# Optimization experiments

Measured on AMD Instinct MI355X. Metric: run time of the kernel, lower is better.

Reference implementation:

```python
import jax, jax.numpy as jnp
import numpy as np

# Mamba config (HF defaults for hidden_size=256)
VOCAB = 4096
H = 256          # hidden_size
I = 512          # intermediate_size = 2*H
N = 16           # state_size
R = 16           # time_step_rank = ceil(H/16)
K = 4            # conv_kernel
NUM_LAYERS = 4
B, L = 4, 1024
EPS = 1e-5


def _rmsnorm(x, w):
    return x * jax.lax.rsqrt(jnp.mean(x * x, axis=-1, keepdims=True) + EPS) * w


def setup_inputs() -> dict:
    key = jax.random.key(0)
    ks = jax.random.split(key, 20)
    s = 0.02
    Lyr = NUM_LAYERS
    inp = {
        'input_ids': jax.random.randint(ks[0], (B, L), 0, VOCAB),
        'lengths': jax.random.randint(ks[1], (B,), 1, L + 1),
        'embed': jax.random.normal(ks[2], (VOCAB, H)) * s,
        'norm_w': jnp.ones((Lyr, H)),
        'in_proj_w': jax.random.normal(ks[3], (Lyr, 2 * I, H)) * s,
        'conv_w': jax.random.normal(ks[4], (Lyr, I, K)) * s,
        'conv_b': jnp.zeros((Lyr, I)),
        'x_proj_w': jax.random.normal(ks[5], (Lyr, R + 2 * N, I)) * s,
        'dt_proj_w': jax.random.normal(ks[6], (Lyr, I, R)) * s,
        'dt_proj_b': jax.random.normal(ks[7], (Lyr, I)) * 0.5 - 4.0,
        'A_log': jnp.log(jnp.broadcast_to(jnp.arange(1, N + 1, dtype=jnp.float32), (Lyr, I, N))),
        'D': jnp.ones((Lyr, I)),
        'out_proj_w': jax.random.normal(ks[8], (Lyr, H, I)) * s,
        'final_norm_w': jnp.ones((H,)),
        'head_w1': jax.random.normal(ks[9], (H // 4, H)) * s,
        'head_b1': jnp.zeros((H // 4,)),
        'head_w2': jax.random.normal(ks[10], (1, H // 4)) * s,
        'head_b2': jnp.zeros((1,)),
    }
    return inp


def _mixer(x, in_proj_w, conv_w, conv_b, x_proj_w, dt_proj_w, dt_proj_b, A_log, D_, out_proj_w):
    b, l, _ = x.shape
    proj = x @ in_proj_w.T                      # (b,l,2I)
    xs, gate = proj[..., :I], proj[..., I:]
    # depthwise causal conv1d (kernel K, left pad K-1)
    xp = jnp.pad(xs, ((0, 0), (K - 1, 0), (0, 0)))
    conv = sum(xp[:, k:k + l, :] * conv_w[:, k] for k in range(K))
    xs = jax.nn.silu(conv + conv_b)             # (b,l,I)
    ssm = xs @ x_proj_w.T                       # (b,l,R+2N)
    dt_r, Bmat, Cmat = ssm[..., :R], ssm[..., R:R + N], ssm[..., R + N:]
    dt = jax.nn.softplus(dt_r @ dt_proj_w.T + dt_proj_b)   # (b,l,I)
    A = -jnp.exp(A_log)                         # (I,N)
    dA = jnp.exp(dt[..., None] * A)             # (b,l,I,N)
    dBu = (dt * xs)[..., None] * Bmat[:, :, None, :]        # (b,l,I,N)

    def step(state, inputs):
        a_t, bu_t, c_t = inputs                 # (b,I,N),(b,I,N),(b,N)
        state = a_t * state + bu_t
        y = jnp.einsum('bdn,bn->bd', state, c_t)
        return state, y

    state0 = jnp.zeros((b, I, N), dtype=x.dtype)
    _, ys = jax.lax.scan(step, state0, (dA.transpose(1, 0, 2, 3),
                                        dBu.transpose(1, 0, 2, 3),
                                        Cmat.transpose(1, 0, 2)))
    ys = ys.transpose(1, 0, 2)                  # (b,l,I)
    y = (ys + xs * D_) * jax.nn.silu(gate)
    return y @ out_proj_w.T                     # (b,l,H)


def reference(input_ids, lengths, embed, norm_w, in_proj_w, conv_w, conv_b,
              x_proj_w, dt_proj_w, dt_proj_b, A_log, D, out_proj_w,
              final_norm_w, head_w1, head_b1, head_w2, head_b2):
    h = embed[input_ids]                        # (B,L,H)
    for i in range(NUM_LAYERS):
        res = h
        x = _rmsnorm(h, norm_w[i])
        h = res + _mixer(x, in_proj_w[i], conv_w[i], conv_b[i], x_proj_w[i],
                         dt_proj_w[i], dt_proj_b[i], A_log[i], D[i], out_proj_w[i])
    h = _rmsnorm(h, final_norm_w)
    pooled = h[jnp.arange(h.shape[0]), lengths - 1]         # (B,H)
    hd = jax.nn.gelu(pooled @ head_w1.T + head_b1, approximate=False)
    out = hd @ head_w2.T + head_b2
    return out.squeeze(-1)                      # (B,)
```

## Files before the change

kernel.cpp:

```cpp
#include <hip/hip_runtime.h>
#include <hip/hip_bf16.h>

#define HDIM 256
#define IDIM 512
#define NST 16
#define KCONV 4
#define LAYERS 4
#define BATCH 4
#define LSEQ 1024
#define TOK (BATCH * LSEQ)

typedef unsigned short u16;
typedef float f32x4 __attribute__((ext_vector_type(4)));
typedef short bf16x8 __attribute__((ext_vector_type(8)));

static __device__ __forceinline__ u16 f2bf(float f) {
    __hip_bfloat16 h = __float2bfloat16(f);
    return reinterpret_cast<u16&>(h);
}
static __device__ __forceinline__ float bf2f(u16 b) {
    return __builtin_bit_cast(float, (unsigned)b << 16);
}
static __device__ __forceinline__ float bfup(uint2 u, int j) {
    unsigned w = (j < 2) ? u.x : u.y;
    unsigned bits = (j & 1) ? (w & 0xffff0000u) : (w << 16);
    return __builtin_bit_cast(float, bits);
}

#define DPP_ROW_ADD(p, CTRL)                                                   \
    p += __builtin_bit_cast(float, __builtin_amdgcn_update_dpp(                \
             0, __builtin_bit_cast(int, p), CTRL, 0xf, 0xf, false))

__global__ __launch_bounds__(256) void embed_kernel(const int* __restrict__ ids,
                                                    const float* __restrict__ embed,
                                                    float* __restrict__ h) {
    int idx = blockIdx.x * 256 + threadIdx.x;
    if (idx < TOK * HDIM) {
        int tok = idx >> 8;
        int c = idx & (HDIM - 1);
        h[idx] = embed[ids[tok] * HDIM + c];
    }
}

__global__ __launch_bounds__(256) void cvt4_bf16_kernel(const float* __restrict__ s0, u16* __restrict__ d0,
                                                        const float* __restrict__ s1, u16* __restrict__ d1,
                                                        const float* __restrict__ s2, u16* __restrict__ d2,
                                                        const float* __restrict__ s3, u16* __restrict__ d3) {
    const float* in;
    u16* out;
    int base;
    int bid = blockIdx.x;
    if (bid < 1024)      { in = s0; out = d0; base = bid; }
    else if (bid < 1536) { in = s1; out = d1; base = bid - 1024; }
    else if (bid < 1632) { in = s2; out = d2; base = bid - 1536; }
    else                 { in = s3; out = d3; base = bid - 1632; }
    int j = (base * 256 + threadIdx.x) * 4;
    float4 v = *(const float4*)&in[j];
    unsigned lo = (unsigned)f2bf(v.x) | ((unsigned)f2bf(v.y) << 16);
    unsigned hi = (unsigned)f2bf(v.z) | ((unsigned)f2bf(v.w) << 16);
    *(uint2*)&out[j] = make_uint2(lo, hi);
}

__global__ __launch_bounds__(256) void rmsnorm_kernel(const float* __restrict__ h,
                                                      const float* __restrict__ w,
                                                      u16* __restrict__ xb) {
    int wid = threadIdx.x >> 6, lane = threadIdx.x & 63;
    int tok = blockIdx.x * 4 + wid;
    float4 v = *(const float4*)&h[(size_t)tok * HDIM + lane * 4];
    float s = v.x * v.x + v.y * v.y + v.z * v.z + v.w * v.w;
    #pragma unroll
    for (int m = 32; m >= 1; m >>= 1) s += __shfl_xor(s, m, 64);
    float rstd = rsqrtf(s * (1.0f / HDIM) + 1e-5f);
    float4 wv = *(const float4*)&w[lane * 4];
    unsigned lo = (unsigned)f2bf(v.x * rstd * wv.x) | ((unsigned)f2bf(v.y * rstd * wv.y) << 16);
    unsigned hi = (unsigned)f2bf(v.z * rstd * wv.z) | ((unsigned)f2bf(v.w * rstd * wv.w) << 16);
    *(uint2*)&xb[(size_t)tok * HDIM + lane * 4] = make_uint2(lo, hi);
}

template <int EPI>
__global__ __launch_bounds__(256) void gemm_bf16_kernel(const u16* __restrict__ A,
                                                        const u16* __restrict__ W,
                                                        float* __restrict__ C,
                                                        int M, int N, int K) {
    const int BM = 128, BK = 32;
    __shared__ __align__(16) u16 Al[BM][BK + 8];
    __shared__ __align__(16) u16 Bl[BM][BK + 8];
    int m0 = blockIdx.y * BM, n0 = blockIdx.x * BM;
    int tid = threadIdx.x;
    int lane = tid & 63;
    int wid = tid >> 6;
    int wr = wid >> 1, wc = wid & 1;
    int r = lane & 15, g = lane >> 4;

    f32x4 acc[4][4] = {};

    int srow = tid & 127;
    const u16* src = (tid < 128) ? (A + (size_t)(m0 + srow) * K)
                                 : (W + (size_t)(n0 + srow) * K);
    u16* dstrow = (tid < 128) ? &Al[srow][0] : &Bl[srow][0];

    for (int k0 = 0; k0 < K; k0 += BK) {
        uint4 v0 = *(const uint4*)(src + k0);
        uint4 v1 = *(const uint4*)(src + k0 + 8);
        uint4 v2 = *(const uint4*)(src + k0 + 16);
        uint4 v3 = *(const uint4*)(src + k0 + 24);
        __syncthreads();
        *(uint4*)(dstrow)      = v0;
        *(uint4*)(dstrow + 8)  = v1;
        *(uint4*)(dstrow + 16) = v2;
        *(uint4*)(dstrow + 24) = v3;
        __syncthreads();

        bf16x8 af[4], bfr[4];
        #pragma unroll
        for (int f = 0; f < 4; ++f) {
            af[f]  = *(const bf16x8*)&Al[wr * 64 + f * 16 + r][g * 8];
            bfr[f] = *(const bf16x8*)&Bl[wc * 64 + f * 16 + r][g * 8];
        }
        #pragma unroll
        for (int fm = 0; fm < 4; ++fm)
            #pragma unroll
            for (int fn = 0; fn < 4; ++fn)
                acc[fm][fn] = __builtin_amdgcn_mfma_f32_16x16x32_bf16(
                    af[fm], bfr[fn], acc[fm][fn], 0, 0, 0);
    }

    #pragma unroll
    for (int fm = 0; fm < 4; ++fm) {
        #pragma unroll
        for (int fn = 0; fn < 4; ++fn) {
            int col = n0 + wc * 64 + fn * 16 + r;
            #pragma unroll
            for (int v = 0; v < 4; ++v) {
                int row = m0 + wr * 64 + fm * 16 + g * 4 + v;
                if (EPI == 1) C[(size_t)row * N + col] += acc[fm][fn][v];
                else          ((u16*)C)[(size_t)row * N + col] = f2bf(acc[fm][fn][v]);
            }
        }
    }
}

__global__ __launch_bounds__(256) void gemm_bf16_n64_kernel(const u16* __restrict__ A,
                                                            const u16* __restrict__ W,
                                                            float* __restrict__ C,
                                                            int M, int N, int K) {
    const int BK = 32;
    __shared__ __align__(16) u16 Al[64][BK + 8];
    __shared__ __align__(16) u16 Bl[64][BK + 8];
    int m0 = blockIdx.y * 64, n0 = blockIdx.x * 64;
    int tid = threadIdx.x;
    int lane = tid & 63;
    int wid = tid >> 6;
    int r = lane & 15, g = lane >> 4;

    f32x4 acc[4] = {};

    int srow = tid & 63;
    const u16* src = (tid < 64) ? (A + (size_t)(m0 + srow) * K)
                                : (W + (size_t)(n0 + srow) * K);
    u16* dstrow = (tid < 64) ? &Al[srow][0] : &Bl[srow][0];

    for (int k0 = 0; k0 < K; k0 += BK) {
        uint4 v0, v1, v2, v3;
        if (tid < 128) {
            v0 = *(const uint4*)(src + k0);
            v1 = *(const uint4*)(src + k0 + 8);
            v2 = *(const uint4*)(src + k0 + 16);
            v3 = *(const uint4*)(src + k0 + 24);
        }
        __syncthreads();
        if (tid < 128) {
            *(uint4*)(dstrow)      = v0;
            *(uint4*)(dstrow + 8)  = v1;
            *(uint4*)(dstrow + 16) = v2;
            *(uint4*)(dstrow + 24) = v3;
        }
        __syncthreads();

        bf16x8 af = *(const bf16x8*)&Al[wid * 16 + r][g * 8];
        #pragma unroll
        for (int fn = 0; fn < 4; ++fn) {
            bf16x8 bfr = *(const bf16x8*)&Bl[fn * 16 + r][g * 8];
            acc[fn] = __builtin_amdgcn_mfma_f32_16x16x32_bf16(af, bfr, acc[fn], 0, 0, 0);
        }
    }

    #pragma unroll
    for (int fn = 0; fn < 4; ++fn) {
        int col = n0 + fn * 16 + r;
        #pragma unroll
        for (int v = 0; v < 4; ++v) {
            int row = m0 + wid * 16 + g * 4 + v;
            C[(size_t)row * N + col] += acc[fn][v];
        }
    }
}

__global__ __launch_bounds__(512) void xproj_kernel(const u16* __restrict__ proj,
                                                    const float* __restrict__ cw,
                                                    const float* __restrict__ cb,
                                                    const u16* __restrict__ W,
                                                    const u16* __restrict__ dtw,
                                                    const float* __restrict__ dtb,
                                                    float* __restrict__ bc,
                                                    float* __restrict__ dtT,
                                                    u16* __restrict__ xs_T,
                                                    u16* __restrict__ gate_T) {
    __shared__ __align__(16) u16 xsL[16][520];
    __shared__ float sP[8][16][52];
    __shared__ float sT[16][52];
    int m0 = blockIdx.x * 16;
    int tid = threadIdx.x;
    int lane = tid & 63;
    int w = tid >> 6;
    int r = lane & 15, g = lane >> 4;
    int tl = m0 & (LSEQ - 1);

    {
        int ic = tid;
        const u16* pxs = proj + (size_t)m0 * 1024 + ic;
        float4 wq = *(const float4*)&cw[ic * 4];
        float bias = cb[ic];
        float a0 = (tl >= 3) ? bf2f(pxs[-3 * 1024]) : 0.f;
        float a1 = (tl >= 2) ? bf2f(pxs[-2 * 1024]) : 0.f;
        float a2 = (tl >= 1) ? bf2f(pxs[-1 * 1024]) : 0.f;
        unsigned xr[8], gr[8];
        #pragma unroll
        for (int t = 0; t < 16; ++t) {
            float a3 = bf2f(pxs[t * 1024]);
            float acc = bias;
            acc = fmaf(a0, wq.x, acc);
            acc = fmaf(a1, wq.y, acc);
            acc = fmaf(a2, wq.z, acc);
            acc = fmaf(a3, wq.w, acc);
            float xsv = acc / (1.f + __expf(-acc));
            u16 xb16 = f2bf(xsv);
            xsL[t][ic] = xb16;
            float gv = bf2f(pxs[t * 1024 + 512]);
            gv = gv / (1.f + __expf(-gv));
            u16 gb16 = f2bf(gv);
            if (t & 1) { xr[t >> 1] |= (unsigned)xb16 << 16; gr[t >> 1] |= (unsigned)gb16 << 16; }
            else       { xr[t >> 1] = xb16;                   gr[t >> 1] = gb16; }
            a0 = a1; a1 = a2; a2 = a3;
        }
        size_t trow = (size_t)ic * TOK + m0;
        *(uint4*)&xs_T[trow]       = make_uint4(xr[0], xr[1], xr[2], xr[3]);
        *(uint4*)&xs_T[trow + 8]   = make_uint4(xr[4], xr[5], xr[6], xr[7]);
        *(uint4*)&gate_T[trow]     = make_uint4(gr[0], gr[1], gr[2], gr[3]);
        *(uint4*)&gate_T[trow + 8] = make_uint4(gr[4], gr[5], gr[6], gr[7]);
    }
    __syncthreads();

    {
        f32x4 acc[3] = {};
        const u16* wbase = W + (size_t)r * 512 + w * 64 + g * 8;
        #pragma unroll
        for (int ks = 0; ks < 2; ++ks) {
            bf16x8 af = *(const bf16x8*)&xsL[r][w * 64 + ks * 32 + g * 8];
            #pragma unroll
            for (int fn = 0; fn < 3; ++fn) {
                bf16x8 bfr = *(const bf16x8*)(wbase + (size_t)fn * 16 * 512 + ks * 32);
                acc[fn] = __builtin_amdgcn_mfma_f32_16x16x32_bf16(af, bfr, acc[fn], 0, 0, 0);
            }
        }
        #pragma unroll
        for (int fn = 0; fn < 3; ++fn)
            #pragma unroll
            for (int v = 0; v < 4; ++v)
                sP[w][g * 4 + v][fn * 16 + r] = acc[fn][v];
    }
    __syncthreads();

    #pragma unroll
    for (int e = 0; e < 2; ++e) {
        int o = tid + e * 512;
        if (o < 768) {
            int row = o / 48, col = o - row * 48;
            float s = 0.f;
            #pragma unroll
            for (int p = 0; p < 8; ++p) s += sP[p][row][col];
            sT[row][col] = s;
        }
    }
    __syncthreads();

    {
        int l = tid;
        int group = l >> 7;
        int rem = l & 127;
        int side = rem >> 6;
        int nn = (rem >> 2) & 15;
        int tq = rem & 3;
        bc[(size_t)blockIdx.x * 512 + l] = sT[group * 4 + tq][16 + side * 16 + nn];
    }

    bf16x8 bv = {};
    if (g < 2) {
        #pragma unroll
        for (int j = 0; j < 8; ++j)
            bv[j] = (short)f2bf(sT[r][g * 8 + j]);
    }
    int mbase = w * 64;
    #pragma unroll
    for (int mf = 0; mf < 4; ++mf) {
        int mrow = mbase + mf * 16;
        bf16x8 av = {};
        if (g < 2) av = *(const bf16x8*)(dtw + (size_t)(mrow + r) * 16 + g * 8);
        f32x4 a2 = __builtin_amdgcn_mfma_f32_16x16x32_bf16(av, bv, f32x4{}, 0, 0, 0);
        float4 b4 = *(const float4*)&dtb[mrow + g * 4];
        #pragma unroll
        for (int v = 0; v < 4; ++v) {
            int i = mrow + g * 4 + v;
            float val = a2[v] + (&b4.x)[v];
            val = fmaxf(val, 0.f) + log1pf(__expf(-fabsf(val)));
            dtT[(size_t)i * TOK + m0 + r] = val;
        }
    }
}

__global__ __launch_bounds__(256, 8) void scan_kernel(const float* __restrict__ dt_T,
                                                      const u16* __restrict__ xs_T,
                                                      const u16* __restrict__ gate_T,
                                                      const float* __restrict__ bc,
                                                      const float* __restrict__ A_log,
                                                      const float* __restrict__ Dw,
                                                      u16* __restrict__ yb) {
    const int NC = 16;
    int n = threadIdx.x & 15;
    int c = threadIdx.x >> 4;

    int lin = (blockIdx.x & 7) * 256 + (blockIdx.x >> 3);
    int b = lin >> 9;
    int i = lin & (IDIM - 1);

    float A = -__expf(A_log[i * NST + n]);

    __shared__ float aprodS[NC][17];
    __shared__ float stendS[NC][17];
    __shared__ float incS[NC][17];

    int t0 = c * 64;
    size_t coff = (size_t)i * TOK + b * LSEQ + t0;
    const float4* dtp = (const float4*)(dt_T + coff);
    const uint2*  xsp = (const uint2*)(xs_T + coff);
    const u16*    xg  = xs_T + coff;
    const u16*    gg  = gate_T + coff;
    const float4* bp  = (const float4*)(bc + (size_t)(b * LSEQ + t0) * 32);

    float aprod = 1.f, st = 0.f;
    #pragma unroll
    for (int q = 0; q < 16; ++q) {
        float4 d4 = dtp[q];
        uint2  xu = xsp[q];
        float4 B4 = __builtin_bit_cast(float4, bp[q * 32 + n]);
        #pragma unroll
        for (int j = 0; j < 4; ++j) {
            float dtv = (&d4.x)[j];
            float dA  = __expf(dtv * A);
            aprod *= dA;
            st = fmaf(dA, st, dtv * bfup(xu, j) * (&B4.x)[j]);
        }
    }
    aprodS[c][n] = aprod;
    stendS[c][n] = st;
    __syncthreads();

    if (threadIdx.x < 16) {
        int nn = threadIdx.x;
        float carry = 0.f;
        for (int cc = 0; cc < NC; ++cc) {
            incS[cc][nn] = carry;
            carry = fmaf(aprodS[cc][nn], carry, stendS[cc][nn]);
        }
    }
    __syncthreads();

    st = incS[c][n];
    float Dv = Dw[i];
    u16* y_b = yb + ((size_t)b * LSEQ + t0) * IDIM + i;
    float yacc = 0.f;

    #pragma unroll 8
    for (int q = 0; q < 16; ++q) {
        float4 d4 = dtp[q];
        uint2  xu = xsp[q];
        float4 B4 = __builtin_bit_cast(float4, bp[q * 32 + n]);
        float4 C4 = __builtin_bit_cast(float4, bp[q * 32 + 16 + n]);
        #pragma unroll
        for (int j = 0; j < 4; ++j) {
            float dtv = (&d4.x)[j];
            float xv  = bfup(xu, j);
            float dA  = __expf(dtv * A);
            st = fmaf(dA, st, dtv * xv * (&B4.x)[j]);
            float py = st * (&C4.x)[j];
            DPP_ROW_ADD(py, 0xB1);
            DPP_ROW_ADD(py, 0x4E);
            DPP_ROW_ADD(py, 0x141);
            DPP_ROW_ADD(py, 0x140);
            yacc = (((q & 3) * 4 + j) == n) ? py : yacc;
        }
        if ((q & 3) == 3) {
            int base = (q - 3) * 4;
            float xvn = bf2f(xg[base + n]);
            float gvn = bf2f(gg[base + n]);
            float yv = fmaf(xvn, Dv, yacc) * gvn;
            y_b[(size_t)(base + n) * IDIM] = f2bf(yv);
        }
    }
}

__global__ __launch_bounds__(256) void head_kernel(const float* __restrict__ h,
                                                   const int* __restrict__ lengths,
                                                   const float* __restrict__ fw,
                                                   const float* __restrict__ w1,
                                                   const float* __restrict__ b1,
                                                   const float* __restrict__ w2,
                                                   const float* __restrict__ b2,
                                                   float* __restrict__ out) {
    int b = blockIdx.x;
    int c = threadIdx.x;
    int len = lengths[b];
    const float* row = h + ((size_t)b * LSEQ + (len - 1)) * HDIM;
    float v = row[c];
    float s = v * v;
    #pragma unroll
    for (int m = 32; m >= 1; m >>= 1) s += __shfl_xor(s, m, 64);
    __shared__ float ls[4];
    __shared__ float pooled[HDIM];
    __shared__ float hd[64];
    if ((c & 63) == 0) ls[c >> 6] = s;
    __syncthreads();
    float tot = ls[0] + ls[1] + ls[2] + ls[3];
    float rstd = rsqrtf(tot * (1.0f / HDIM) + 1e-5f);
    pooled[c] = v * rstd * fw[c];
    __syncthreads();
    if (c < 64) {
        float a = b1[c];
        for (int k = 0; k < HDIM; ++k) a = fmaf(pooled[k], w1[c * HDIM + k], a);
        float g = 0.5f * a * (1.f + erff(a * 0.70710678118654752f));
        hd[c] = g * w2[c];
    }
    __syncthreads();
    if (c == 0) {
        float o = b2[0];
        for (int k = 0; k < 64; ++k) o += hd[k];
        out[b] = o;
    }
}

extern "C" void kernel_launch(void* const* d_in, const int* in_sizes, int n_in,
                              void* d_out, int out_size, void* d_ws, size_t ws_size,
                              hipStream_t stream) {
    const int*   ids         = (const int*)d_in[0];
    const int*   lengths     = (const int*)d_in[1];
    const float* embed       = (const float*)d_in[2];
    const float* norm_w      = (const float*)d_in[3];
    const float* in_proj_w   = (const float*)d_in[4];
    const float* conv_w      = (const float*)d_in[5];
    const float* conv_b      = (const float*)d_in[6];
    const float* x_proj_w    = (const float*)d_in[7];
    const float* dt_proj_w   = (const float*)d_in[8];
    const float* dt_proj_b   = (const float*)d_in[9];
    const float* A_log       = (const float*)d_in[10];
    const float* Dw          = (const float*)d_in[11];
    const float* out_proj_w  = (const float*)d_in[12];
    const float* final_norm_w= (const float*)d_in[13];
    const float* head_w1     = (const float*)d_in[14];
    const float* head_b1     = (const float*)d_in[15];
    const float* head_w2     = (const float*)d_in[16];
    const float* head_b2     = (const float*)d_in[17];

    float* ws   = (float*)d_ws;
    float* h    = ws;
    float* dtT  = h    + 1048576;
    float* bc   = dtT  + 2097152;
    u16* xb   = (u16*)(bc + 131072);
    u16* yb   = xb   + 1048576;
    u16* wib  = yb   + 2097152;
    u16* wob  = wib  + 1048576;
    u16* xwb  = wob  + 524288;
    u16* dtwb = xwb  + 98304;
    u16* projb= dtwb + 32768;
    u16* xsT  = projb+ 4194304;
    u16* gT   = xsT  + 2097152;

    embed_kernel<<<TOK * HDIM / 256, 256, 0, stream>>>(ids, embed, h);
    cvt4_bf16_kernel<<<1664, 256, 0, stream>>>(in_proj_w, wib, out_proj_w, wob,
                                               x_proj_w, xwb, dt_proj_w, dtwb);

    for (int l = 0; l < LAYERS; ++l) {
        rmsnorm_kernel<<<TOK / 4, 256, 0, stream>>>(h, norm_w + l * HDIM, xb);
        gemm_bf16_kernel<2><<<dim3(1024 / 128, TOK / 128), 256, 0, stream>>>(
            xb, wib + (size_t)l * 2 * IDIM * HDIM, (float*)projb, TOK, 2 * IDIM, HDIM);
        xproj_kernel<<<TOK / 16, 512, 0, stream>>>(
            projb, conv_w + l * IDIM * KCONV, conv_b + l * IDIM,
            xwb + (size_t)l * 48 * IDIM, dtwb + (size_t)l * IDIM * 16,
            dt_proj_b + l * IDIM, bc, dtT, xsT, gT);
        scan_kernel<<<BATCH * IDIM, 256, 0, stream>>>(
            dtT, xsT, gT, bc, A_log + (size_t)l * IDIM * NST, Dw + l * IDIM, yb);
        gemm_bf16_n64_kernel<<<dim3(HDIM / 64, TOK / 64), 256, 0, stream>>>(
            yb, wob + (size_t)l * HDIM * IDIM, h, TOK, HDIM, IDIM);
    }

    head_kernel<<<BATCH, 256, 0, stream>>>(h, lengths, final_norm_w,
                                           head_w1, head_b1, head_w2, head_b2,
                                           (float*)d_out);
}
```

Baseline: 338.1 us.

## Fuse out-projection residual add with next layer RMSNorm

Replaces the tiled out-projection GEMM with a kernel that computes full 16-row strips across all 256 columns, reading operands directly from global memory without LDS staging. It adds the result into the residual stream and then computes the next layer's RMSNorm in the same kernel, removing the separate per-layer rmsnorm launch and one re-read of h. The scan kernel's occupancy hint is also lowered from 8 to 4 blocks per CU. Risks: the direct global loads of W are repeated for every block without LDS reuse. Writing xb with final_norm_w on the last layer is unused but harmless.

```diff
diff --git a/kernel.cpp b/kernel.cpp
--- a/kernel.cpp
+++ b/kernel.cpp
@@ -77,10 +77,9 @@
     *(uint2*)&xb[(size_t)tok * HDIM + lane * 4] = make_uint2(lo, hi);
 }
 
-template <int EPI>
 __global__ __launch_bounds__(256) void gemm_bf16_kernel(const u16* __restrict__ A,
                                                         const u16* __restrict__ W,
-                                                        float* __restrict__ C,
+                                                        u16* __restrict__ C,
                                                         int M, int N, int K) {
     const int BM = 128, BK = 32;
     __shared__ __align__(16) u16 Al[BM][BK + 8];
@@ -133,67 +132,72 @@
             #pragma unroll
             for (int v = 0; v < 4; ++v) {
                 int row = m0 + wr * 64 + fm * 16 + g * 4 + v;
-                if (EPI == 1) C[(size_t)row * N + col] += acc[fm][fn][v];
-                else          ((u16*)C)[(size_t)row * N + col] = f2bf(acc[fm][fn][v]);
+                C[(size_t)row * N + col] = f2bf(acc[fm][fn][v]);
             }
         }
     }
 }
 
-__global__ __launch_bounds__(256) void gemm_bf16_n64_kernel(const u16* __restrict__ A,
-                                                            const u16* __restrict__ W,
-                                                            float* __restrict__ C,
-                                                            int M, int N, int K) {
-    const int BK = 32;
-    __shared__ __align__(16) u16 Al[64][BK + 8];
-    __shared__ __align__(16) u16 Bl[64][BK + 8];
-    int m0 = blockIdx.y * 64, n0 = blockIdx.x * 64;
+__global__ __launch_bounds__(256) void outproj_norm_kernel(const u16* __restrict__ Y,
+                                                           const u16* __restrict__ W,
+                                                           const float* __restrict__ nw,
+                                                           float* __restrict__ h,
+                                                           u16* __restrict__ xb) {
+    __shared__ float sH[16][260];
+    int m0 = blockIdx.x * 16;
     int tid = threadIdx.x;
     int lane = tid & 63;
-    int wid = tid >> 6;
+    int w = tid >> 6;
     int r = lane & 15, g = lane >> 4;
 
     f32x4 acc[4] = {};
-
-    int srow = tid & 63;
-    const u16* src = (tid < 64) ? (A + (size_t)(m0 + srow) * K)
-                                : (W + (size_t)(n0 + srow) * K);
-    u16* dstrow = (tid < 64) ? &Al[srow][0] : &Bl[srow][0];
-
-    for (int k0 = 0; k0 < K; k0 += BK) {
-        uint4 v0, v1, v2, v3;
-        if (tid < 128) {
-            v0 = *(const uint4*)(src + k0);
-            v1 = *(const uint4*)(src + k0 + 8);
-            v2 = *(const uint4*)(src + k0 + 16);
-            v3 = *(const uint4*)(src + k0 + 24);
-        }
-        __syncthreads();
-        if (tid < 128) {
-            *(uint4*)(dstrow)      = v0;
-            *(uint4*)(dstrow + 8)  = v1;
-            *(uint4*)(dstrow + 16) = v2;
-            *(uint4*)(dstrow + 24) = v3;
-        }
-        __syncthreads();
-
-        bf16x8 af = *(const bf16x8*)&Al[wid * 16 + r][g * 8];
+    const u16* yrow  = Y + (size_t)(m0 + r) * 512 + g * 8;
+    const u16* wbase = W + (size_t)(w * 64 + r) * 512 + g * 8;
+    #pragma unroll
+    for (int k0 = 0; k0 < 512; k0 += 32) {
+        bf16x8 af = *(const bf16x8*)(yrow + k0);
         #pragma unroll
         for (int fn = 0; fn < 4; ++fn) {
-            bf16x8 bfr = *(const bf16x8*)&Bl[fn * 16 + r][g * 8];
+            bf16x8 bfr = *(const bf16x8*)(wbase + (size_t)fn * 16 * 512 + k0);
             acc[fn] = __builtin_amdgcn_mfma_f32_16x16x32_bf16(af, bfr, acc[fn], 0, 0, 0);
         }
     }
 
     #pragma unroll
     for (int fn = 0; fn < 4; ++fn) {
-        int col = n0 + fn * 16 + r;
+        int col = w * 64 + fn * 16 + r;
         #pragma unroll
         for (int v = 0; v < 4; ++v) {
-            int row = m0 + wid * 16 + g * 4 + v;
-            C[(size_t)row * N + col] += acc[fn][v];
-        }
-    }
+            int row = g * 4 + v;
+            size_t off = (size_t)(m0 + row) * HDIM + col;
+            float hv = h[off] + acc[fn][v];
+            h[off] = hv;
+            sH[row][col] = hv;
+        }
+    }
+    __syncthreads();
+
+    int row = tid >> 4, part = tid & 15;
+    const float* sr = &sH[row][part * 16];
+    float s = 0.f;
+    #pragma unroll
+    for (int j = 0; j < 16; ++j) s = fmaf(sr[j], sr[j], s);
+    DPP_ROW_ADD(s, 0xB1);
+    DPP_ROW_ADD(s, 0x4E);
+    DPP_ROW_ADD(s, 0x141);
+    DPP_ROW_ADD(s, 0x140);
+    float rstd = rsqrtf(s * (1.0f / HDIM) + 1e-5f);
+    const float* nwp = &nw[part * 16];
+    unsigned pk[8];
+    #pragma unroll
+    for (int j = 0; j < 8; ++j) {
+        u16 lo = f2bf(sr[2 * j]     * rstd * nwp[2 * j]);
+        u16 hi = f2bf(sr[2 * j + 1] * rstd * nwp[2 * j + 1]);
+        pk[j] = (unsigned)lo | ((unsigned)hi << 16);
+    }
+    u16* dst = xb + (size_t)(m0 + row) * HDIM + part * 16;
+    *(uint4*)(dst)     = make_uint4(pk[0], pk[1], pk[2], pk[3]);
+    *(uint4*)(dst + 8) = make_uint4(pk[4], pk[5], pk[6], pk[7]);
 }
 
 __global__ __launch_bounds__(512) void xproj_kernel(const u16* __restrict__ proj,
@@ -318,7 +322,7 @@
     }
 }
 
-__global__ __launch_bounds__(256, 8) void scan_kernel(const float* __restrict__ dt_T,
+__global__ __launch_bounds__(256, 4) void scan_kernel(const float* __restrict__ dt_T,
                                                       const u16* __restrict__ xs_T,
                                                       const u16* __restrict__ gate_T,
                                                       const float* __restrict__ bc,
@@ -487,19 +491,20 @@
     embed_kernel<<<TOK * HDIM / 256, 256, 0, stream>>>(ids, embed, h);
     cvt4_bf16_kernel<<<1664, 256, 0, stream>>>(in_proj_w, wib, out_proj_w, wob,
                                                x_proj_w, xwb, dt_proj_w, dtwb);
+    rmsnorm_kernel<<<TOK / 4, 256, 0, stream>>>(h, norm_w, xb);
 
     for (int l = 0; l < LAYERS; ++l) {
-        rmsnorm_kernel<<<TOK / 4, 256, 0, stream>>>(h, norm_w + l * HDIM, xb);
-        gemm_bf16_kernel<2><<<dim3(1024 / 128, TOK / 128), 256, 0, stream>>>(
-            xb, wib + (size_t)l * 2 * IDIM * HDIM, (float*)projb, TOK, 2 * IDIM, HDIM);
+        gemm_bf16_kernel<<<dim3(1024 / 128, TOK / 128), 256, 0, stream>>>(
+            xb, wib + (size_t)l * 2 * IDIM * HDIM, projb, TOK, 2 * IDIM, HDIM);
         xproj_kernel<<<TOK / 16, 512, 0, stream>>>(
             projb, conv_w + l * IDIM * KCONV, conv_b + l * IDIM,
             xwb + (size_t)l * 48 * IDIM, dtwb + (size_t)l * IDIM * 16,
             dt_proj_b + l * IDIM, bc, dtT, xsT, gT);
         scan_kernel<<<BATCH * IDIM, 256, 0, stream>>>(
             dtT, xsT, gT, bc, A_log + (size_t)l * IDIM * NST, Dw + l * IDIM, yb);
-        gemm_bf16_n64_kernel<<<dim3(HDIM / 64, TOK / 64), 256, 0, stream>>>(
-            yb, wob + (size_t)l * HDIM * IDIM, h, TOK, HDIM, IDIM);
+        const float* nw_next = (l + 1 < LAYERS) ? (norm_w + (l + 1) * HDIM) : final_norm_w;
+        outproj_norm_kernel<<<TOK / 16, 256, 0, stream>>>(
+            yb, wob + (size_t)l * HDIM * IDIM, nw_next, h, xb);
     }
 
     head_kernel<<<BATCH, 256, 0, stream>>>(h, lengths, final_norm_w,
```

Measured after the change: 314.9 us. 6.9% less time.
